# Performance work log

Measured on AMD Instinct MI355X. Metric: run time of the kernel, lower is better.

Reference implementation:

```python
import jax, jax.numpy as jnp
import numpy as np

B, N, QD = 2, 4096, 512
HEADS, DIM_HEAD = 8, 64
INNER = HEADS * DIM_HEAD  # 512
SCALE = DIM_HEAD ** -0.5


def setup_inputs() -> dict:
    key = jax.random.key(0)
    ks = jax.random.split(key, 6)
    s = 0.02
    return {
        "x": jax.random.normal(ks[0], (B, N, QD), dtype=jnp.float32),
        "Wq": jax.random.normal(ks[1], (QD, INNER), dtype=jnp.float32) * s,
        "Wk": jax.random.normal(ks[2], (QD, INNER), dtype=jnp.float32) * s,
        "Wv": jax.random.normal(ks[3], (QD, INNER), dtype=jnp.float32) * s,
        "Wo": jax.random.normal(ks[4], (INNER, QD), dtype=jnp.float32) * s,
        "bo": jnp.zeros((QD,), dtype=jnp.float32),
    }


def reference(x, Wq, Wk, Wv, Wo, bo):
    # self-attention: context = x; mask = None; attention_sf = False
    q = x @ Wq  # [B, N, INNER]
    k = x @ Wk
    v = x @ Wv
    # split heads: [B, H, N, D]
    def split(t):
        return t.reshape(B, N, HEADS, DIM_HEAD).transpose(0, 2, 1, 3)
    q, k, v = split(q), split(k), split(v)
    # fp32 QK^T (ATTN_PRECISION='fp32' path)
    sim = jnp.einsum('bhid,bhjd->bhij', q.astype(jnp.float32), k.astype(jnp.float32)) * SCALE
    attn = jax.nn.softmax(sim, axis=-1)
    out = jnp.einsum('bhij,bhjd->bhid', attn, v)  # [B, H, N, D]
    out = out.transpose(0, 2, 1, 3).reshape(B, N, INNER)
    return out @ Wo + bo  # Dropout(p=0) is identity
```

## Files before the change

### kernel.cpp

```cpp
#include <hip/hip_runtime.h>
#include <hip/hip_bf16.h>


typedef __attribute__((ext_vector_type(8))) short short8;
typedef __attribute__((ext_vector_type(4))) float floatx4;

#define MFMA16(a, b, c) __builtin_amdgcn_mfma_f32_16x16x32_bf16((a), (b), (c), 0, 0, 0)

#if __has_builtin(__builtin_amdgcn_exp2f)
#define EXP2(x) __builtin_amdgcn_exp2f(x)
#else
#define EXP2(x) exp2f(x)
#endif

#define QSCALE 0.18033688011112042f

static __device__ __forceinline__ unsigned short f2b(float f) {
  unsigned int u = __float_as_uint(f);
  u += 0x7FFFu + ((u >> 16) & 1u);
  return (unsigned short)(u >> 16);
}

static __device__ __forceinline__ unsigned int pkb(float a, float b) {
  float2 t{a, b};
  __hip_bfloat162 h = __float22bfloat162_rn(t);
  union { __hip_bfloat162 h2; unsigned int u; } cv;
  cv.h2 = h;
  return cv.u;
}

__global__ __launch_bounds__(256) void wt_cvt_kernel(
    const float* __restrict__ Wq, const float* __restrict__ Wk,
    const float* __restrict__ Wv, const float* __restrict__ Wo,
    unsigned short* __restrict__ wtq, unsigned short* __restrict__ wtk,
    unsigned short* __restrict__ wtv, unsigned short* __restrict__ wto) {
  const int z = blockIdx.z;
  const float* __restrict__ W = (z == 0) ? Wq : (z == 1) ? Wk : (z == 2) ? Wv : Wo;
  unsigned short* __restrict__ T = (z == 0) ? wtq : (z == 1) ? wtk : (z == 2) ? wtv : wto;
  const int k0 = blockIdx.x * 32, c0 = blockIdx.y * 32;
  __shared__ float Ts[32][33];
  const int tid = threadIdx.x;
  const int r = tid >> 3, cc = (tid & 7) * 4;
  const float4 v = *(const float4*)(W + (k0 + r) * 512 + c0 + cc);
  Ts[r][cc] = v.x; Ts[r][cc + 1] = v.y; Ts[r][cc + 2] = v.z; Ts[r][cc + 3] = v.w;
  __syncthreads();
  const unsigned long long uu =
      (unsigned long long)pkb(Ts[cc][r], Ts[cc + 1][r]) |
      ((unsigned long long)pkb(Ts[cc + 2][r], Ts[cc + 3][r]) << 32);
  *(unsigned long long*)(T + (c0 + r) * 512 + k0 + cc) = uu;
}

__global__ __launch_bounds__(256) void qkv_proj_kernel(
    const float* __restrict__ x, const unsigned short* __restrict__ wtq,
    const unsigned short* __restrict__ wtk,
    const unsigned short* __restrict__ wtv, unsigned short* __restrict__ qo,
    unsigned short* __restrict__ ko, unsigned short* __restrict__ vo) {
  const int m0 = blockIdx.x * 64;
  const int c0 = blockIdx.y * 64;
  __shared__ __align__(16) unsigned short As[64 * 40];
  __shared__ __align__(16) unsigned short Bs[3][64 * 40];
  const int tid = threadIdx.x;
  const int lane = tid & 63, wvid = tid >> 6;
  const int i = lane & 15, q = lane >> 4;
  const int wy = wvid >> 1, wx = wvid & 1;
  const int arow = tid >> 2, acol = (tid & 3) * 8;
  floatx4 acc[3][2][2] = {};
  for (int k0 = 0; k0 < 512; k0 += 32) {
    __syncthreads();
    {
      const float* src = x + (m0 + arow) * 512 + k0 + acol;
      short8 av;
#pragma unroll
      for (int j = 0; j < 8; ++j) av[j] = (short)f2b(src[j]);
      *(short8*)&As[arow * 40 + acol] = av;
    }
    *(short8*)&Bs[0][arow * 40 + acol] =
        *(const short8*)(wtq + (c0 + arow) * 512 + k0 + acol);
    *(short8*)&Bs[1][arow * 40 + acol] =
        *(const short8*)(wtk + (c0 + arow) * 512 + k0 + acol);
    *(short8*)&Bs[2][arow * 40 + acol] =
        *(const short8*)(wtv + (c0 + arow) * 512 + k0 + acol);
    __syncthreads();
    short8 af[2];
#pragma unroll
    for (int t = 0; t < 2; ++t)
      af[t] = *(const short8*)&As[(wy * 32 + t * 16 + i) * 40 + q * 8];
#pragma unroll
    for (int z = 0; z < 3; ++z)
#pragma unroll
      for (int g = 0; g < 2; ++g) {
        const short8 bf =
            *(const short8*)&Bs[z][(wx * 32 + g * 16 + i) * 40 + q * 8];
#pragma unroll
        for (int t = 0; t < 2; ++t) acc[z][t][g] = MFMA16(af[t], bf, acc[z][t][g]);
      }
  }
#pragma unroll
  for (int z = 0; z < 3; ++z)
#pragma unroll
    for (int t = 0; t < 2; ++t)
#pragma unroll
      for (int g = 0; g < 2; ++g) {
        const int col = c0 + wx * 32 + g * 16 + i;
        const int h = col >> 6, d = col & 63;
        const int row0 = m0 + wy * 32 + t * 16 + q * 4;
        const int b = row0 >> 12;
        const int n0 = row0 & 4095;
        if (z == 2) {
          unsigned int* dst =
              (unsigned int*)&vo[(((b * 8 + h) * 64 + d) << 12) + n0];
          dst[0] = pkb(acc[z][t][g][0], acc[z][t][g][1]);
          dst[1] = pkb(acc[z][t][g][2], acc[z][t][g][3]);
        } else {
          unsigned short* dst = (z == 0) ? qo : ko;
          const float sc = (z == 0) ? QSCALE : 1.0f;
#pragma unroll
          for (int r = 0; r < 4; ++r)
            dst[(((b * 8 + h) << 12) + (n0 + r)) * 64 + d] =
                f2b(acc[z][t][g][r] * sc);
        }
      }
}

__global__ __launch_bounds__(512, 4) void flash_kernel(
    const unsigned short* __restrict__ Q, const unsigned short* __restrict__ K,
    const unsigned short* __restrict__ Vt, unsigned short* __restrict__ O) {
  const int bh = blockIdx.x;
  const int m0 = blockIdx.y * 128;
  const int tid = threadIdx.x;
  const int lane = tid & 63, w = tid >> 6;
  const int i = lane & 15, q = lane >> 4;
  const int rt = w & 3;
  const int kg = w >> 2;
  const unsigned short* qp = Q + bh * (4096 * 64);
  const unsigned short* kp = K + bh * (4096 * 64);
  const unsigned short* vp = Vt + bh * (64 * 4096);

  __shared__ __align__(16) unsigned short SM[32768];
  unsigned short* Ks = SM + kg * 4096;
  unsigned short* Vs = SM + 8192 + kg * 4096;
  unsigned short* pw = SM + 16384 + w * 2048;

  const int srow = (tid & 255) >> 3;
  const int c0s = tid & 7;
  const int sw8 = (c0s ^ (srow & 7)) * 8;
  const unsigned short* kgp = kp + (kg * 2048 + srow) * 64 + c0s * 8;
  const unsigned short* vgp = vp + srow * 4096 + kg * 2048 + c0s * 8;

  short8 qf[2][2];
#pragma unroll
  for (int t = 0; t < 2; ++t)
#pragma unroll
    for (int kc = 0; kc < 2; ++kc)
      qf[t][kc] = *(const short8*)(qp + (m0 + rt * 32 + t * 16 + i) * 64 +
                                   kc * 32 + q * 8);

  floatx4 accO[2][4] = {};
  floatx4 accL[2] = {};
  short8 ones;
  {
    const short ov = (i == 0) ? (short)0x3F80 : (short)0;
#pragma unroll
    for (int j = 0; j < 8; ++j) ones[j] = ov;
  }
  const floatx4 zf = {0.f, 0.f, 0.f, 0.f};

  const int sl = i & 7;

  *(short8*)&Ks[srow * 64 + sw8] = *(const short8*)(kgp);
  *(short8*)&Ks[(srow + 32) * 64 + sw8] = *(const short8*)(kgp + 32 * 64);
  *(short8*)&Vs[srow * 64 + sw8] = *(const short8*)(vgp);
  *(short8*)&Vs[(srow + 32) * 64 + sw8] = *(const short8*)(vgp + 32 * 4096);
  __syncthreads();

  for (int jt = 0; jt < 32; ++jt) {
    short8 kn0, kn1, vn0, vn1;
    if (jt < 31) {
      kn0 = *(const short8*)(kgp + (jt + 1) * 4096);
      kn1 = *(const short8*)(kgp + (jt + 1) * 4096 + 32 * 64);
      vn0 = *(const short8*)(vgp + (jt + 1) * 64);
      vn1 = *(const short8*)(vgp + (jt + 1) * 64 + 32 * 4096);
    }
#pragma unroll
    for (int g = 0; g < 4; ++g) {
      const short8 kf0 = *(const short8*)(&Ks[(g * 16 + i) * 64 + (q ^ sl) * 8]);
      const short8 kf1 =
          *(const short8*)(&Ks[(g * 16 + i) * 64 + ((4 + q) ^ sl) * 8]);
#pragma unroll
      for (int t = 0; t < 2; ++t) {
        floatx4 s = MFMA16(kf0, qf[t][0], zf);
        s = MFMA16(kf1, qf[t][1], s);
        const float e0 = EXP2(s[0]), e1 = EXP2(s[1]);
        const float e2 = EXP2(s[2]), e3 = EXP2(s[3]);
        *(unsigned long long*)&pw[(t * 16 + i) * 64 +
                                  (((2 * g + (q >> 1)) ^ sl) * 8) +
                                  (q & 1) * 4] =
            (unsigned long long)pkb(e0, e1) |
            ((unsigned long long)pkb(e2, e3) << 32);
      }
    }
    short8 pf[2][2];
#pragma unroll
    for (int t = 0; t < 2; ++t) {
      pf[t][0] = *(const short8*)(pw + (t * 16 + i) * 64 + (q ^ sl) * 8);
      pf[t][1] = *(const short8*)(pw + (t * 16 + i) * 64 + ((4 + q) ^ sl) * 8);
      accL[t] = MFMA16(pf[t][0], ones, accL[t]);
      accL[t] = MFMA16(pf[t][1], ones, accL[t]);
    }
#pragma unroll
    for (int dg = 0; dg < 4; ++dg) {
      const short8 vf0 =
          *(const short8*)(&Vs[(dg * 16 + i) * 64 + (q ^ sl) * 8]);
      const short8 vf1 =
          *(const short8*)(&Vs[(dg * 16 + i) * 64 + ((4 + q) ^ sl) * 8]);
#pragma unroll
      for (int t = 0; t < 2; ++t) {
        accO[t][dg] = MFMA16(pf[t][0], vf0, accO[t][dg]);
        accO[t][dg] = MFMA16(pf[t][1], vf1, accO[t][dg]);
      }
    }
    __syncthreads();
    if (jt < 31) {
      *(short8*)&Ks[srow * 64 + sw8] = kn0;
      *(short8*)&Ks[(srow + 32) * 64 + sw8] = kn1;
      *(short8*)&Vs[srow * 64 + sw8] = vn0;
      *(short8*)&Vs[(srow + 32) * 64 + sw8] = vn1;
    }
    __syncthreads();
  }

  float* MB = (float*)SM;
  if (kg == 1) {
    float* dst = MB + (rt * 64 + lane) * 40;
#pragma unroll
    for (int t = 0; t < 2; ++t) {
#pragma unroll
      for (int dg = 0; dg < 4; ++dg)
#pragma unroll
        for (int r = 0; r < 4; ++r) dst[t * 16 + dg * 4 + r] = accO[t][dg][r];
#pragma unroll
      for (int r = 0; r < 4; ++r) dst[32 + t * 4 + r] = accL[t][r];
    }
  }
  __syncthreads();
  if (kg == 1) return;
  {
    const float* src = MB + (rt * 64 + lane) * 40;
#pragma unroll
    for (int t = 0; t < 2; ++t) {
#pragma unroll
      for (int dg = 0; dg < 4; ++dg)
#pragma unroll
        for (int r = 0; r < 4; ++r) accO[t][dg][r] += src[t * 16 + dg * 4 + r];
#pragma unroll
      for (int r = 0; r < 4; ++r) accL[t][r] += src[32 + t * 4 + r];
    }
  }

  const int b = bh >> 3, h = bh & 7;
#pragma unroll
  for (int t = 0; t < 2; ++t) {
    float inv[4];
#pragma unroll
    for (int r = 0; r < 4; ++r) {
      const float l = __shfl(accL[t][r], lane & 48, 64);
      inv[r] = 1.0f / l;
    }
#pragma unroll
    for (int dg = 0; dg < 4; ++dg)
#pragma unroll
      for (int r = 0; r < 4; ++r) {
        const int n = m0 + rt * 32 + t * 16 + q * 4 + r;
        const int col = h * 64 + dg * 16 + i;
        O[((b << 12) + n) * 512 + col] = f2b(accO[t][dg][r] * inv[r]);
      }
  }
}

__global__ __launch_bounds__(256) void out_proj_kernel(
    const unsigned short* __restrict__ A, const unsigned short* __restrict__ wto,
    const float* __restrict__ bo, float* __restrict__ out) {
  const int m0 = blockIdx.x * 64, c0 = blockIdx.y * 64;
  __shared__ __align__(16) unsigned short As[64 * 40];
  __shared__ __align__(16) unsigned short Bs[64 * 40];
  const int tid = threadIdx.x;
  const int lane = tid & 63, wvid = tid >> 6;
  const int i = lane & 15, q = lane >> 4;
  const int wy = wvid >> 1, wx = wvid & 1;
  const int arow = tid >> 2, acol = (tid & 3) * 8;
  floatx4 acc[2][2] = {};
  for (int k0 = 0; k0 < 512; k0 += 32) {
    __syncthreads();
    *(short8*)&As[arow * 40 + acol] =
        *(const short8*)(A + (m0 + arow) * 512 + k0 + acol);
    *(short8*)&Bs[arow * 40 + acol] =
        *(const short8*)(wto + (c0 + arow) * 512 + k0 + acol);
    __syncthreads();
    short8 af[2], bfr[2];
#pragma unroll
    for (int t = 0; t < 2; ++t)
      af[t] = *(const short8*)&As[(wy * 32 + t * 16 + i) * 40 + q * 8];
#pragma unroll
    for (int g = 0; g < 2; ++g)
      bfr[g] = *(const short8*)&Bs[(wx * 32 + g * 16 + i) * 40 + q * 8];
#pragma unroll
    for (int t = 0; t < 2; ++t)
#pragma unroll
      for (int g = 0; g < 2; ++g) acc[t][g] = MFMA16(af[t], bfr[g], acc[t][g]);
  }
#pragma unroll
  for (int t = 0; t < 2; ++t)
#pragma unroll
    for (int g = 0; g < 2; ++g) {
      const int col = c0 + wx * 32 + g * 16 + i;
      const float bias = bo[col];
#pragma unroll
      for (int r = 0; r < 4; ++r) {
        const int row = m0 + wy * 32 + t * 16 + q * 4 + r;
        out[row * 512 + col] = acc[t][g][r] + bias;
      }
    }
}

extern "C" void kernel_launch(void* const* d_in, const int* in_sizes, int n_in,
                              void* d_out, int out_size, void* d_ws,
                              size_t ws_size, hipStream_t stream) {
  const float* x = (const float*)d_in[0];
  const float* Wq = (const float*)d_in[1];
  const float* Wk = (const float*)d_in[2];
  const float* Wv = (const float*)d_in[3];
  const float* Wo = (const float*)d_in[4];
  const float* bo = (const float*)d_in[5];
  float* out = (float*)d_out;

  const size_t tsz = (size_t)16 * 4096 * 64;
  unsigned short* qws = (unsigned short*)d_ws;
  unsigned short* kws = qws + tsz;
  unsigned short* vws = kws + tsz;
  unsigned short* ows = vws + tsz;
  unsigned short* wtq = ows + tsz;
  unsigned short* wtk = wtq + 512 * 512;
  unsigned short* wtv = wtk + 512 * 512;
  unsigned short* wto = wtv + 512 * 512;

  wt_cvt_kernel<<<dim3(16, 16, 4), 256, 0, stream>>>(Wq, Wk, Wv, Wo, wtq, wtk,
                                                     wtv, wto);
  qkv_proj_kernel<<<dim3(128, 8), 256, 0, stream>>>(x, wtq, wtk, wtv, qws, kws,
                                                    vws);
  flash_kernel<<<dim3(16, 32), 512, 0, stream>>>(qws, kws, vws, ows);
  out_proj_kernel<<<dim3(128, 8), 256, 0, stream>>>(ows, wto, bo, out);
}
```

Baseline: 197.9 us.

## Split attention KV range across four waves per 64-row query block

Restructures the flash kernel from 512-thread blocks (4 row tiles x 2 KV groups over 128 query rows) to 256-thread blocks where each wave owns all 64 query rows and a quarter of the key sequence, using 32-key sub-tiles per wave. The grid becomes 64x16 blocks and LDS use drops, which should allow more resident blocks and reuse each K/V fragment across four query tiles. In exchange, the final reduction now serially combines three waves' partial accumulators through shared memory with extra barriers, and per-wave register pressure grows with the larger accO.

```diff
diff --git a/kernel.cpp b/kernel.cpp
--- a/kernel.cpp
+++ b/kernel.cpp
@@ -122,41 +122,41 @@
       }
 }
 
-__global__ __launch_bounds__(512, 4) void flash_kernel(
+__global__ __launch_bounds__(256, 4) void flash_kernel(
     const unsigned short* __restrict__ Q, const unsigned short* __restrict__ K,
     const unsigned short* __restrict__ Vt, unsigned short* __restrict__ O) {
-  const int bh = blockIdx.x;
-  const int m0 = blockIdx.y * 128;
+  const int m0 = blockIdx.x * 64;
+  const int bh = blockIdx.y;
   const int tid = threadIdx.x;
   const int lane = tid & 63, w = tid >> 6;
   const int i = lane & 15, q = lane >> 4;
-  const int rt = w & 3;
-  const int kg = w >> 2;
+  const int sl7 = i & 7, sl3 = i & 3;
   const unsigned short* qp = Q + bh * (4096 * 64);
   const unsigned short* kp = K + bh * (4096 * 64);
   const unsigned short* vp = Vt + bh * (64 * 4096);
 
-  __shared__ __align__(16) unsigned short SM[32768];
-  unsigned short* Ks = SM + kg * 4096;
-  unsigned short* Vs = SM + 8192 + kg * 4096;
-  unsigned short* pw = SM + 16384 + w * 2048;
-
-  const int srow = (tid & 255) >> 3;
-  const int c0s = tid & 7;
-  const int sw8 = (c0s ^ (srow & 7)) * 8;
-  const unsigned short* kgp = kp + (kg * 2048 + srow) * 64 + c0s * 8;
-  const unsigned short* vgp = vp + srow * 4096 + kg * 2048 + c0s * 8;
-
-  short8 qf[2][2];
-#pragma unroll
-  for (int t = 0; t < 2; ++t)
+  __shared__ __align__(16) unsigned short SM[18432];
+  unsigned short* Ks = SM + w * 2048;
+  unsigned short* Vs = SM + 8192 + w * 2048;
+  unsigned short* pw = SM + 16384 + w * 512;
+
+  const int ksr = lane >> 3, ksc = lane & 7;
+  const unsigned short* kgl = kp + (w * 1024 + ksr) * 64 + ksc * 8;
+  const int kdo = ksr * 64 + ((ksc ^ ksr) * 8);
+  const int vsr = lane >> 2, vsc = lane & 3;
+  const unsigned short* vgl = vp + vsr * 4096 + w * 1024 + vsc * 8;
+  const int vdo = vsr * 32 + ((vsc ^ (vsr & 3)) * 8);
+
+  short8 qf[4][2];
+#pragma unroll
+  for (int t = 0; t < 4; ++t)
 #pragma unroll
     for (int kc = 0; kc < 2; ++kc)
-      qf[t][kc] = *(const short8*)(qp + (m0 + rt * 32 + t * 16 + i) * 64 +
-                                   kc * 32 + q * 8);
-
-  floatx4 accO[2][4] = {};
-  floatx4 accL[2] = {};
+      qf[t][kc] =
+          *(const short8*)(qp + (m0 + t * 16 + i) * 64 + kc * 32 + q * 8);
+
+  floatx4 accO[4][4] = {};
+  floatx4 accL[4] = {};
   short8 ones;
   {
     const short ov = (i == 0) ? (short)0x3F80 : (short)0;
@@ -165,101 +165,92 @@
   }
   const floatx4 zf = {0.f, 0.f, 0.f, 0.f};
 
-  const int sl = i & 7;
-
-  *(short8*)&Ks[srow * 64 + sw8] = *(const short8*)(kgp);
-  *(short8*)&Ks[(srow + 32) * 64 + sw8] = *(const short8*)(kgp + 32 * 64);
-  *(short8*)&Vs[srow * 64 + sw8] = *(const short8*)(vgp);
-  *(short8*)&Vs[(srow + 32) * 64 + sw8] = *(const short8*)(vgp + 32 * 4096);
+#pragma unroll
+  for (int p = 0; p < 4; ++p) {
+    *(short8*)&Ks[p * 512 + kdo] = *(const short8*)(kgl + p * 512);
+    *(short8*)&Vs[p * 512 + vdo] = *(const short8*)(vgl + p * 65536);
+  }
   __syncthreads();
 
   for (int jt = 0; jt < 32; ++jt) {
-    short8 kn0, kn1, vn0, vn1;
+    short8 kn[4], vn[4];
     if (jt < 31) {
-      kn0 = *(const short8*)(kgp + (jt + 1) * 4096);
-      kn1 = *(const short8*)(kgp + (jt + 1) * 4096 + 32 * 64);
-      vn0 = *(const short8*)(vgp + (jt + 1) * 64);
-      vn1 = *(const short8*)(vgp + (jt + 1) * 64 + 32 * 4096);
-    }
-#pragma unroll
-    for (int g = 0; g < 4; ++g) {
-      const short8 kf0 = *(const short8*)(&Ks[(g * 16 + i) * 64 + (q ^ sl) * 8]);
-      const short8 kf1 =
-          *(const short8*)(&Ks[(g * 16 + i) * 64 + ((4 + q) ^ sl) * 8]);
-#pragma unroll
-      for (int t = 0; t < 2; ++t) {
-        floatx4 s = MFMA16(kf0, qf[t][0], zf);
-        s = MFMA16(kf1, qf[t][1], s);
+#pragma unroll
+      for (int p = 0; p < 4; ++p) {
+        kn[p] = *(const short8*)(kgl + (jt + 1) * 2048 + p * 512);
+        vn[p] = *(const short8*)(vgl + (jt + 1) * 32 + p * 65536);
+      }
+    }
+    short8 kf[2][2], vf[4];
+#pragma unroll
+    for (int g = 0; g < 2; ++g)
+#pragma unroll
+      for (int kc = 0; kc < 2; ++kc)
+        kf[g][kc] =
+            *(const short8*)&Ks[(g * 16 + i) * 64 + (((kc * 4 + q) ^ sl7) * 8)];
+#pragma unroll
+    for (int dg = 0; dg < 4; ++dg)
+      vf[dg] = *(const short8*)&Vs[(dg * 16 + i) * 32 + ((q ^ sl3) * 8)];
+
+#pragma unroll
+    for (int t = 0; t < 4; ++t) {
+#pragma unroll
+      for (int g = 0; g < 2; ++g) {
+        floatx4 s = MFMA16(kf[g][0], qf[t][0], zf);
+        s = MFMA16(kf[g][1], qf[t][1], s);
         const float e0 = EXP2(s[0]), e1 = EXP2(s[1]);
         const float e2 = EXP2(s[2]), e3 = EXP2(s[3]);
-        *(unsigned long long*)&pw[(t * 16 + i) * 64 +
-                                  (((2 * g + (q >> 1)) ^ sl) * 8) +
+        *(unsigned long long*)&pw[i * 32 + (((2 * g + (q >> 1)) ^ sl3) * 8) +
                                   (q & 1) * 4] =
             (unsigned long long)pkb(e0, e1) |
             ((unsigned long long)pkb(e2, e3) << 32);
       }
-    }
-    short8 pf[2][2];
-#pragma unroll
-    for (int t = 0; t < 2; ++t) {
-      pf[t][0] = *(const short8*)(pw + (t * 16 + i) * 64 + (q ^ sl) * 8);
-      pf[t][1] = *(const short8*)(pw + (t * 16 + i) * 64 + ((4 + q) ^ sl) * 8);
-      accL[t] = MFMA16(pf[t][0], ones, accL[t]);
-      accL[t] = MFMA16(pf[t][1], ones, accL[t]);
-    }
-#pragma unroll
-    for (int dg = 0; dg < 4; ++dg) {
-      const short8 vf0 =
-          *(const short8*)(&Vs[(dg * 16 + i) * 64 + (q ^ sl) * 8]);
-      const short8 vf1 =
-          *(const short8*)(&Vs[(dg * 16 + i) * 64 + ((4 + q) ^ sl) * 8]);
-#pragma unroll
-      for (int t = 0; t < 2; ++t) {
-        accO[t][dg] = MFMA16(pf[t][0], vf0, accO[t][dg]);
-        accO[t][dg] = MFMA16(pf[t][1], vf1, accO[t][dg]);
-      }
+      const short8 pf = *(const short8*)&pw[i * 32 + ((q ^ sl3) * 8)];
+      accL[t] = MFMA16(pf, ones, accL[t]);
+#pragma unroll
+      for (int dg = 0; dg < 4; ++dg)
+        accO[t][dg] = MFMA16(pf, vf[dg], accO[t][dg]);
     }
     __syncthreads();
     if (jt < 31) {
-      *(short8*)&Ks[srow * 64 + sw8] = kn0;
-      *(short8*)&Ks[(srow + 32) * 64 + sw8] = kn1;
-      *(short8*)&Vs[srow * 64 + sw8] = vn0;
-      *(short8*)&Vs[(srow + 32) * 64 + sw8] = vn1;
-    }
-    __syncthreads();
-  }
-
-  float* MB = (float*)SM;
-  if (kg == 1) {
-    float* dst = MB + (rt * 64 + lane) * 40;
-#pragma unroll
-    for (int t = 0; t < 2; ++t) {
-#pragma unroll
-      for (int dg = 0; dg < 4; ++dg)
-#pragma unroll
-        for (int r = 0; r < 4; ++r) dst[t * 16 + dg * 4 + r] = accO[t][dg][r];
-#pragma unroll
-      for (int r = 0; r < 4; ++r) dst[32 + t * 4 + r] = accL[t][r];
-    }
-  }
-  __syncthreads();
-  if (kg == 1) return;
-  {
-    const float* src = MB + (rt * 64 + lane) * 40;
-#pragma unroll
-    for (int t = 0; t < 2; ++t) {
-#pragma unroll
-      for (int dg = 0; dg < 4; ++dg)
-#pragma unroll
-        for (int r = 0; r < 4; ++r) accO[t][dg][r] += src[t * 16 + dg * 4 + r];
-#pragma unroll
-      for (int r = 0; r < 4; ++r) accL[t][r] += src[32 + t * 4 + r];
-    }
-  }
+#pragma unroll
+      for (int p = 0; p < 4; ++p) {
+        *(short8*)&Ks[p * 512 + kdo] = kn[p];
+        *(short8*)&Vs[p * 512 + vdo] = vn[p];
+      }
+    }
+    __syncthreads();
+  }
+
+  floatx4* MB = (floatx4*)SM;
+#pragma unroll
+  for (int r = 1; r < 4; ++r) {
+    if (w == r) {
+#pragma unroll
+      for (int t = 0; t < 4; ++t) {
+#pragma unroll
+        for (int dg = 0; dg < 4; ++dg)
+          MB[(t * 4 + dg) * 64 + lane] = accO[t][dg];
+        MB[(16 + t) * 64 + lane] = accL[t];
+      }
+    }
+    __syncthreads();
+    if (w == 0) {
+#pragma unroll
+      for (int t = 0; t < 4; ++t) {
+#pragma unroll
+        for (int dg = 0; dg < 4; ++dg)
+          accO[t][dg] += MB[(t * 4 + dg) * 64 + lane];
+        accL[t] += MB[(16 + t) * 64 + lane];
+      }
+    }
+    __syncthreads();
+  }
+  if (w != 0) return;
 
   const int b = bh >> 3, h = bh & 7;
 #pragma unroll
-  for (int t = 0; t < 2; ++t) {
+  for (int t = 0; t < 4; ++t) {
     float inv[4];
 #pragma unroll
     for (int r = 0; r < 4; ++r) {
@@ -270,7 +261,7 @@
     for (int dg = 0; dg < 4; ++dg)
 #pragma unroll
       for (int r = 0; r < 4; ++r) {
-        const int n = m0 + rt * 32 + t * 16 + q * 4 + r;
+        const int n = m0 + t * 16 + q * 4 + r;
         const int col = h * 64 + dg * 16 + i;
         O[((b << 12) + n) * 512 + col] = f2b(accO[t][dg][r] * inv[r]);
       }
@@ -347,6 +338,6 @@
                                                      wtv, wto);
   qkv_proj_kernel<<<dim3(128, 8), 256, 0, stream>>>(x, wtq, wtk, wtv, qws, kws,
                                                     vws);
-  flash_kernel<<<dim3(16, 32), 512, 0, stream>>>(qws, kws, vws, ows);
+  flash_kernel<<<dim3(64, 16), 256, 0, stream>>>(qws, kws, vws, ows);
   out_proj_kernel<<<dim3(128, 8), 256, 0, stream>>>(ows, wto, bo, out);
 }
```

Result: slower. 595.8 us (+201.1%).

## Pre-convert x to bf16 and use direct global-to-LDS loads in projection GEMMs

Applied to the files above, without the earlier changes.

Adds a separate kernel that converts x to bf16 once, so the QKV projection no longer converts fp32 to bf16 inside its tile loop. The QKV GEMM is restructured into 128x128 tiles with one weight matrix per grid z-slice. Both the QKV and output projections now stage tiles through global_load_lds DMA into unpadded LDS instead of register round-trips. This trades an extra launch and a workspace round-trip for x, plus possible LDS bank conflicts from dropping the padding, for less per-tile staging work and more data reuse per block.

```diff
diff --git a/kernel.cpp b/kernel.cpp
--- a/kernel.cpp
+++ b/kernel.cpp
@@ -27,6 +27,13 @@
   union { __hip_bfloat162 h2; unsigned int u; } cv;
   cv.h2 = h;
   return cv.u;
+}
+
+static __device__ __forceinline__ void dma16(const unsigned short* g,
+                                             unsigned short* l) {
+  __builtin_amdgcn_global_load_lds(
+      (const __attribute__((address_space(1))) unsigned int*)g,
+      (__attribute__((address_space(3))) unsigned int*)l, 16, 0, 0);
 }
 
 __global__ __launch_bounds__(256) void wt_cvt_kernel(
@@ -50,76 +57,81 @@
   *(unsigned long long*)(T + (c0 + r) * 512 + k0 + cc) = uu;
 }
 
+__global__ __launch_bounds__(256) void x_cvt_kernel(
+    const float* __restrict__ x, unsigned short* __restrict__ xb) {
+  const int idx = (blockIdx.x * 256 + threadIdx.x) * 8;
+  const float4 a = *(const float4*)(x + idx);
+  const float4 b = *(const float4*)(x + idx + 4);
+  unsigned int u[4] = {pkb(a.x, a.y), pkb(a.z, a.w), pkb(b.x, b.y),
+                       pkb(b.z, b.w)};
+  *(short8*)(xb + idx) = *(short8*)u;
+}
+
 __global__ __launch_bounds__(256) void qkv_proj_kernel(
-    const float* __restrict__ x, const unsigned short* __restrict__ wtq,
+    const unsigned short* __restrict__ xb, const unsigned short* __restrict__ wtq,
     const unsigned short* __restrict__ wtk,
     const unsigned short* __restrict__ wtv, unsigned short* __restrict__ qo,
     unsigned short* __restrict__ ko, unsigned short* __restrict__ vo) {
-  const int m0 = blockIdx.x * 64;
-  const int c0 = blockIdx.y * 64;
-  __shared__ __align__(16) unsigned short As[64 * 40];
-  __shared__ __align__(16) unsigned short Bs[3][64 * 40];
+  const int z = blockIdx.z;
+  const unsigned short* __restrict__ wt = (z == 0) ? wtq : (z == 1) ? wtk : wtv;
+  const int m0 = blockIdx.x * 128;
+  const int c0 = blockIdx.y * 128;
+  __shared__ __align__(16) unsigned short As[128 * 32];
+  __shared__ __align__(16) unsigned short Bs[128 * 32];
   const int tid = threadIdx.x;
-  const int lane = tid & 63, wvid = tid >> 6;
+  const int lane = tid & 63, w = tid >> 6;
   const int i = lane & 15, q = lane >> 4;
-  const int wy = wvid >> 1, wx = wvid & 1;
-  const int arow = tid >> 2, acol = (tid & 3) * 8;
-  floatx4 acc[3][2][2] = {};
+  const int wy = w >> 1, wx = w & 1;
+  const int sr = lane >> 2, sc8 = (lane & 3) * 8;
+  const unsigned short* ag = xb + (m0 + w * 32 + sr) * 512 + sc8;
+  const unsigned short* bg = wt + (c0 + w * 32 + sr) * 512 + sc8;
+  unsigned short* adst0 = &As[(w * 32) * 32];
+  unsigned short* adst1 = &As[(w * 32 + 16) * 32];
+  unsigned short* bdst0 = &Bs[(w * 32) * 32];
+  unsigned short* bdst1 = &Bs[(w * 32 + 16) * 32];
+  floatx4 acc[4][4] = {};
   for (int k0 = 0; k0 < 512; k0 += 32) {
-    __syncthreads();
-    {
-      const float* src = x + (m0 + arow) * 512 + k0 + acol;
-      short8 av;
-#pragma unroll
-      for (int j = 0; j < 8; ++j) av[j] = (short)f2b(src[j]);
-      *(short8*)&As[arow * 40 + acol] = av;
-    }
-    *(short8*)&Bs[0][arow * 40 + acol] =
-        *(const short8*)(wtq + (c0 + arow) * 512 + k0 + acol);
-    *(short8*)&Bs[1][arow * 40 + acol] =
-        *(const short8*)(wtk + (c0 + arow) * 512 + k0 + acol);
-    *(short8*)&Bs[2][arow * 40 + acol] =
-        *(const short8*)(wtv + (c0 + arow) * 512 + k0 + acol);
-    __syncthreads();
-    short8 af[2];
-#pragma unroll
-    for (int t = 0; t < 2; ++t)
-      af[t] = *(const short8*)&As[(wy * 32 + t * 16 + i) * 40 + q * 8];
-#pragma unroll
-    for (int z = 0; z < 3; ++z)
-#pragma unroll
-      for (int g = 0; g < 2; ++g) {
-        const short8 bf =
-            *(const short8*)&Bs[z][(wx * 32 + g * 16 + i) * 40 + q * 8];
-#pragma unroll
-        for (int t = 0; t < 2; ++t) acc[z][t][g] = MFMA16(af[t], bf, acc[z][t][g]);
-      }
-  }
-#pragma unroll
-  for (int z = 0; z < 3; ++z)
-#pragma unroll
-    for (int t = 0; t < 2; ++t)
-#pragma unroll
-      for (int g = 0; g < 2; ++g) {
-        const int col = c0 + wx * 32 + g * 16 + i;
-        const int h = col >> 6, d = col & 63;
-        const int row0 = m0 + wy * 32 + t * 16 + q * 4;
-        const int b = row0 >> 12;
-        const int n0 = row0 & 4095;
-        if (z == 2) {
-          unsigned int* dst =
-              (unsigned int*)&vo[(((b * 8 + h) * 64 + d) << 12) + n0];
-          dst[0] = pkb(acc[z][t][g][0], acc[z][t][g][1]);
-          dst[1] = pkb(acc[z][t][g][2], acc[z][t][g][3]);
-        } else {
-          unsigned short* dst = (z == 0) ? qo : ko;
-          const float sc = (z == 0) ? QSCALE : 1.0f;
-#pragma unroll
-          for (int r = 0; r < 4; ++r)
-            dst[(((b * 8 + h) << 12) + (n0 + r)) * 64 + d] =
-                f2b(acc[z][t][g][r] * sc);
-        }
-      }
+    dma16(ag + k0, adst0);
+    dma16(ag + 16 * 512 + k0, adst1);
+    dma16(bg + k0, bdst0);
+    dma16(bg + 16 * 512 + k0, bdst1);
+    __syncthreads();
+    short8 af[4], bfr[4];
+#pragma unroll
+    for (int t = 0; t < 4; ++t)
+      af[t] = *(const short8*)&As[(wy * 64 + t * 16 + i) * 32 + q * 8];
+#pragma unroll
+    for (int g = 0; g < 4; ++g)
+      bfr[g] = *(const short8*)&Bs[(wx * 64 + g * 16 + i) * 32 + q * 8];
+#pragma unroll
+    for (int t = 0; t < 4; ++t)
+#pragma unroll
+      for (int g = 0; g < 4; ++g) acc[t][g] = MFMA16(af[t], bfr[g], acc[t][g]);
+    __syncthreads();
+  }
+#pragma unroll
+  for (int t = 0; t < 4; ++t)
+#pragma unroll
+    for (int g = 0; g < 4; ++g) {
+      const int col = c0 + wx * 64 + g * 16 + i;
+      const int h = col >> 6, d = col & 63;
+      const int row0 = m0 + wy * 64 + t * 16 + q * 4;
+      const int b = row0 >> 12;
+      const int n0 = row0 & 4095;
+      if (z == 2) {
+        unsigned int* dst =
+            (unsigned int*)&vo[(((b * 8 + h) * 64 + d) << 12) + n0];
+        dst[0] = pkb(acc[t][g][0], acc[t][g][1]);
+        dst[1] = pkb(acc[t][g][2], acc[t][g][3]);
+      } else {
+        unsigned short* dst = (z == 0) ? qo : ko;
+        const float sc = (z == 0) ? QSCALE : 1.0f;
+#pragma unroll
+        for (int r = 0; r < 4; ++r)
+          dst[(((b * 8 + h) << 12) + (n0 + r)) * 64 + d] =
+              f2b(acc[t][g][r] * sc);
+      }
+    }
 }
 
 __global__ __launch_bounds__(512, 4) void flash_kernel(
@@ -164,7 +176,6 @@
     for (int j = 0; j < 8; ++j) ones[j] = ov;
   }
   const floatx4 zf = {0.f, 0.f, 0.f, 0.f};
-
   const int sl = i & 7;
 
   *(short8*)&Ks[srow * 64 + sw8] = *(const short8*)(kgp);
@@ -281,32 +292,34 @@
     const unsigned short* __restrict__ A, const unsigned short* __restrict__ wto,
     const float* __restrict__ bo, float* __restrict__ out) {
   const int m0 = blockIdx.x * 64, c0 = blockIdx.y * 64;
-  __shared__ __align__(16) unsigned short As[64 * 40];
-  __shared__ __align__(16) unsigned short Bs[64 * 40];
+  __shared__ __align__(16) unsigned short As[64 * 32];
+  __shared__ __align__(16) unsigned short Bs[64 * 32];
   const int tid = threadIdx.x;
-  const int lane = tid & 63, wvid = tid >> 6;
+  const int lane = tid & 63, w = tid >> 6;
   const int i = lane & 15, q = lane >> 4;
-  const int wy = wvid >> 1, wx = wvid & 1;
-  const int arow = tid >> 2, acol = (tid & 3) * 8;
+  const int wy = w >> 1, wx = w & 1;
+  const int sr = lane >> 2, sc8 = (lane & 3) * 8;
+  const unsigned short* ag = A + (m0 + w * 16 + sr) * 512 + sc8;
+  const unsigned short* bg = wto + (c0 + w * 16 + sr) * 512 + sc8;
+  unsigned short* adst = &As[(w * 16) * 32];
+  unsigned short* bdst = &Bs[(w * 16) * 32];
   floatx4 acc[2][2] = {};
   for (int k0 = 0; k0 < 512; k0 += 32) {
-    __syncthreads();
-    *(short8*)&As[arow * 40 + acol] =
-        *(const short8*)(A + (m0 + arow) * 512 + k0 + acol);
-    *(short8*)&Bs[arow * 40 + acol] =
-        *(const short8*)(wto + (c0 + arow) * 512 + k0 + acol);
+    dma16(ag + k0, adst);
+    dma16(bg + k0, bdst);
     __syncthreads();
     short8 af[2], bfr[2];
 #pragma unroll
     for (int t = 0; t < 2; ++t)
-      af[t] = *(const short8*)&As[(wy * 32 + t * 16 + i) * 40 + q * 8];
+      af[t] = *(const short8*)&As[(wy * 32 + t * 16 + i) * 32 + q * 8];
 #pragma unroll
     for (int g = 0; g < 2; ++g)
-      bfr[g] = *(const short8*)&Bs[(wx * 32 + g * 16 + i) * 40 + q * 8];
+      bfr[g] = *(const short8*)&Bs[(wx * 32 + g * 16 + i) * 32 + q * 8];
 #pragma unroll
     for (int t = 0; t < 2; ++t)
 #pragma unroll
       for (int g = 0; g < 2; ++g) acc[t][g] = MFMA16(af[t], bfr[g], acc[t][g]);
+    __syncthreads();
   }
 #pragma unroll
   for (int t = 0; t < 2; ++t)
@@ -342,11 +355,13 @@
   unsigned short* wtk = wtq + 512 * 512;
   unsigned short* wtv = wtk + 512 * 512;
   unsigned short* wto = wtv + 512 * 512;
+  unsigned short* xb = wto + 512 * 512;
 
   wt_cvt_kernel<<<dim3(16, 16, 4), 256, 0, stream>>>(Wq, Wk, Wv, Wo, wtq, wtk,
                                                      wtv, wto);
-  qkv_proj_kernel<<<dim3(128, 8), 256, 0, stream>>>(x, wtq, wtk, wtv, qws, kws,
-                                                    vws);
+  x_cvt_kernel<<<2048, 256, 0, stream>>>(x, xb);
+  qkv_proj_kernel<<<dim3(64, 4, 3), 256, 0, stream>>>(xb, wtq, wtk, wtv, qws,
+                                                      kws, vws);
   flash_kernel<<<dim3(16, 32), 512, 0, stream>>>(qws, kws, vws, ows);
   out_proj_kernel<<<dim3(128, 8), 256, 0, stream>>>(ows, wto, bo, out);
 }
```

Result: no change. 198.0 us (+0.1%).
